# Optimization experiments

Hardware: AMD Instinct MI355X
Metric: run time of the kernel (lower is better)

## Reference

```python
import jax, jax.numpy as jnp
import numpy as np
from jax import lax

N, C, H, W = 16, 1024, 32, 32
CQK = C // 8
EPS = 1e-5


def setup_inputs() -> dict:
    key = jax.random.key(0)
    ks = jax.random.split(key, 10)
    s = lambda fan_in: 1.0 / np.sqrt(fan_in)
    return {
        "x": jax.random.normal(ks[0], (N, C, H, W), dtype=jnp.float32),
        "head_w": jax.random.uniform(ks[1], (1, C, 3, 3), jnp.float32, -s(C * 9), s(C * 9)),
        "bn_w": jnp.ones((1,), jnp.float32),
        "bn_b": jnp.zeros((1,), jnp.float32),
        "q_w": jax.random.uniform(ks[2], (CQK, C), jnp.float32, -s(C), s(C)),
        "q_b": jax.random.uniform(ks[3], (CQK,), jnp.float32, -s(C), s(C)),
        "k_w": jax.random.uniform(ks[4], (CQK, C), jnp.float32, -s(C), s(C)),
        "k_b": jax.random.uniform(ks[5], (CQK,), jnp.float32, -s(C), s(C)),
        "v_w": jax.random.uniform(ks[6], (C, C), jnp.float32, -s(C), s(C)),
        "v_b": jax.random.uniform(ks[7], (C,), jnp.float32, -s(C), s(C)),
        "gamma": jnp.ones((1,), jnp.float32),
    }


def reference(x, head_w, bn_w, bn_b, q_w, q_b, k_w, k_b, v_w, v_b, gamma):
    n, c, h, w = x.shape
    hw = h * w
    # activation head: 3x3 conv (no bias) -> BatchNorm (train mode, batch stats) -> sigmoid
    a = lax.conv_general_dilated(x, head_w, (1, 1), ((1, 1), (1, 1)),
                                 dimension_numbers=("NCHW", "OIHW", "NCHW"))  # [n,1,h,w]
    mu = jnp.mean(a, axis=(0, 2, 3), keepdims=True)
    var = jnp.mean((a - mu) ** 2, axis=(0, 2, 3), keepdims=True)
    bn = (a - mu) / jnp.sqrt(var + EPS) * bn_w.reshape(1, -1, 1, 1) + bn_b.reshape(1, -1, 1, 1)
    ccam = jax.nn.sigmoid(bn)  # [n,1,h,w]

    xf = x.reshape(n, c, hw)                 # [n,c,hw]
    cm = ccam.reshape(n, hw)                 # [n,hw]
    fg = jnp.einsum("nh,nch->nc", cm, xf) / hw
    bg = jnp.einsum("nh,nch->nc", 1.0 - cm, xf) / hw

    # self-attention with 1x1-conv projections (no 1/sqrt(d) scaling, per source)
    q = jnp.einsum("oc,nch->noh", q_w, xf) + q_b[None, :, None]  # [n,cqk,hw]
    k = jnp.einsum("oc,nch->noh", k_w, xf) + k_b[None, :, None]
    v = jnp.einsum("oc,nch->noh", v_w, xf) + v_b[None, :, None]  # [n,c,hw]
    attn = jax.nn.softmax(jnp.einsum("noi,noj->nij", q, k), axis=-1)  # [n,hw,hw]
    out = jnp.einsum("ncj,nij->nci", v, attn)                         # [n,c,hw]
    out = gamma * out + xf

    global_feats = jnp.max(out, axis=-1)  # adaptive_max_pool2d to (1,1)
    return fg, bg, ccam, global_feats
```

## Files before the change

### kernel.cpp

```cpp
#include <hip/hip_runtime.h>
#include <math.h>

typedef _Float16 f16x8 __attribute__((ext_vector_type(8)));
typedef float f32x4 __attribute__((ext_vector_type(4)));

#define NB 16
#define CC 1024
#define HW 1024
#define CQK 128
#define EPS 1e-5f

#define OFF_A     0
#define OFF_STATS 65536
#define OFF_CM    66048
#define OFF_WH    131584
#define OFF_QT    (OFF_WH + 2621440)
#define OFF_KT    (OFF_QT + 4194304)
#define OFF_V     (OFF_KT + 4194304)
#define OFF_XH    (OFF_V + 33554432)
#define OFF_ATTN  OFF_XH
#define OFF_PMAX  (OFF_ATTN + 67108864)
#define OFF_YP    OFF_V

__device__ __forceinline__ ushort f16b(float f) {
    union { _Float16 h; ushort u; } v;
    v.h = (_Float16)f;
    return v.u;
}

__device__ __forceinline__ void gl_lds16(const void* g, void* s) {
    __builtin_amdgcn_global_load_lds(
        (const __attribute__((address_space(1))) void*)g,
        (__attribute__((address_space(3))) void*)s, 16, 0, 0);
}

__global__ __launch_bounds__(256) void cvtT_x_conv(
        const float* __restrict__ x, const float* __restrict__ hwt,
        ushort* __restrict__ xh, float* __restrict__ yp) {
    int n = blockIdx.z, cb = blockIdx.y, hb = blockIdx.x;
    __shared__ float tile[32][33];
    int t = threadIdx.x;
    int r = t >> 3, c4 = (t & 7) << 2;
    const float* s = x + ((size_t)(n * CC + cb * 32 + r) << 10) + hb * 32 + c4;
    float4 v = *(const float4*)s;
    tile[r][c4] = v.x; tile[r][c4 + 1] = v.y; tile[r][c4 + 2] = v.z; tile[r][c4 + 3] = v.w;
    __syncthreads();
    int hw_l = t >> 3, cg = (t & 7) << 2;
    ushort4 h4;
    h4.x = f16b(tile[cg + 0][hw_l]); h4.y = f16b(tile[cg + 1][hw_l]);
    h4.z = f16b(tile[cg + 2][hw_l]); h4.w = f16b(tile[cg + 3][hw_l]);
    *(ushort4*)&xh[((size_t)(n * HW + hb * 32 + hw_l) << 10) + cb * 32 + cg] = h4;
    float pacc[9] = {};
    #pragma unroll
    for (int cc = 0; cc < 4; ++cc) {
        float xv = tile[cg + cc][hw_l];
        const float* w9 = hwt + (cb * 32 + cg + cc) * 9;
        #pragma unroll
        for (int tp = 0; tp < 9; ++tp) pacc[tp] += xv * w9[tp];
    }
    #pragma unroll
    for (int off = 1; off < 8; off <<= 1)
        #pragma unroll
        for (int tp = 0; tp < 9; ++tp) pacc[tp] += __shfl_xor(pacc[tp], off);
    if ((t & 7) == 0) {
        #pragma unroll
        for (int tp = 0; tp < 9; ++tp)
            yp[(((size_t)(n * 32 + cb) * 9 + tp) << 10) + hb * 32 + hw_l] = pacc[tp];
    }
}

__global__ __launch_bounds__(256) void conv_combine(
        const float* __restrict__ yp, float* __restrict__ a) {
    int idx = blockIdx.x * 256 + threadIdx.x;
    int n = idx >> 10, p = idx & 1023;
    int h = p >> 5, w = p & 31;
    float s = 0.f;
    #pragma unroll
    for (int tp = 0; tp < 9; ++tp) {
        int dy = tp / 3 - 1, dx = tp % 3 - 1;
        int hh = h + dy, ww = w + dx;
        if (hh < 0 || hh > 31 || ww < 0 || ww > 31) continue;
        int pp = (hh << 5) + ww;
        const float* b = yp + (((size_t)(n * 32) * 9) << 10) + ((size_t)tp << 10) + pp;
        #pragma unroll
        for (int cch = 0; cch < 32; ++cch) s += b[((size_t)cch * 9) << 10];
    }
    a[idx] = s;
}

__global__ void bn_stats(const float* __restrict__ a, float* __restrict__ stats) {
    int t = threadIdx.x;
    float s = 0.f, ss = 0.f;
    for (int i = t; i < NB * HW; i += 256) { float v = a[i]; s += v; ss += v * v; }
    __shared__ float rs[256], rss[256];
    rs[t] = s; rss[t] = ss;
    __syncthreads();
    for (int off = 128; off > 0; off >>= 1) {
        if (t < off) { rs[t] += rs[t + off]; rss[t] += rss[t + off]; }
        __syncthreads();
    }
    if (t == 0) {
        float mu = rs[0] / (NB * HW);
        float var = rss[0] / (NB * HW) - mu * mu;
        stats[0] = mu;
        stats[1] = rsqrtf(var + EPS);
    }
}

__global__ void ccam_kernel(const float* __restrict__ a, const float* __restrict__ stats,
                            const float* __restrict__ bn_w, const float* __restrict__ bn_b,
                            float* __restrict__ cm, float* __restrict__ out_ccam) {
    int i = blockIdx.x * 256 + threadIdx.x;
    float z = (a[i] - stats[0]) * stats[1] * bn_w[0] + bn_b[0];
    float sg = 1.f / (1.f + expf(-z));
    cm[i] = sg;
    out_ccam[i] = sg;
}

__global__ void fgbg_kernel(const float* __restrict__ x, const float* __restrict__ cm,
                            float* __restrict__ out_fg, float* __restrict__ out_bg) {
    int gid = blockIdx.x * blockDim.x + threadIdx.x;
    int wid = gid >> 6;
    int lane = threadIdx.x & 63;
    int n = wid >> 10, c = wid & 1023;
    const float4* xp = (const float4*)(x + ((size_t)(n * CC + c) << 10));
    const float4* cp = (const float4*)(cm + (n << 10));
    float sf = 0.f, sa = 0.f;
    #pragma unroll
    for (int it = 0; it < 4; ++it) {
        float4 xv = xp[lane + (it << 6)];
        float4 cv = cp[lane + (it << 6)];
        sf += xv.x * cv.x + xv.y * cv.y + xv.z * cv.z + xv.w * cv.w;
        sa += xv.x + xv.y + xv.z + xv.w;
    }
    for (int off = 32; off > 0; off >>= 1) { sf += __shfl_xor(sf, off); sa += __shfl_xor(sa, off); }
    if (lane == 0) {
        float fgv = sf * (1.f / HW);
        out_fg[(n << 10) + c] = fgv;
        out_bg[(n << 10) + c] = sa * (1.f / HW) - fgv;
    }
}

__global__ void cvt_w(const float* __restrict__ qw, const float* __restrict__ kw,
                      const float* __restrict__ vw, ushort* __restrict__ wh) {
    size_t e = ((size_t)blockIdx.x * 256 + threadIdx.x) * 4;
    float4 v;
    if (e < 131072)       v = *(const float4*)(qw + e);
    else if (e < 262144)  v = *(const float4*)(kw + e - 131072);
    else                  v = *(const float4*)(vw + e - 262144);
    ushort4 h4;
    h4.x = f16b(v.x); h4.y = f16b(v.y); h4.z = f16b(v.z); h4.w = f16b(v.w);
    *(ushort4*)&wh[e] = h4;
}

__device__ __forceinline__ void gemm_loop_f16(
        const ushort* __restrict__ Ag, int ap,
        const ushort* __restrict__ Bg, int bp,
        int K, ushort* lds, f32x4 acc[4][4]) {
    const int t = threadIdx.x;
    const int lane = t & 63, w = t >> 6;
    const int lr = lane & 15, kg = lane >> 4;
    const int wm = (w >> 1) << 6, wn = (w & 1) << 6;
    const int rowl = lane >> 3;
    const int cs = (lane & 7) ^ rowl;
    const ushort* sA = Ag + cs * 8;
    const ushort* sB = Bg + cs * 8;
    const int rb = (w << 3) + rowl;
    const int ldsb = w << 9;
    const int cA0 = kg ^ (lr & 7);
    const int cA1 = (kg | 4) ^ (lr & 7);
    const int nt = K >> 6;
    #pragma unroll
    for (int q = 0; q < 4; ++q) {
        int r = rb + (q << 5);
        gl_lds16(sA + (size_t)r * ap, lds + ldsb + (q << 11));
        gl_lds16(sB + (size_t)r * bp, lds + 8192 + ldsb + (q << 11));
    }
    __syncthreads();
    int buf = 0;
    for (int tile = 0; tile < nt; ++tile) {
        if (tile + 1 < nt) {
            int nb = (buf ^ 1) << 14;
            int k0 = (tile + 1) << 6;
            #pragma unroll
            for (int q = 0; q < 4; ++q) {
                int r = rb + (q << 5);
                gl_lds16(sA + (size_t)r * ap + k0, lds + nb + ldsb + (q << 11));
                gl_lds16(sB + (size_t)r * bp + k0, lds + nb + 8192 + ldsb + (q << 11));
            }
        }
        const ushort* Ab = lds + (buf << 14);
        const ushort* Bb = Ab + 8192;
        #pragma unroll
        for (int s = 0; s < 2; ++s) {
            int ch = s ? cA1 : cA0;
            f16x8 a[4], b[4];
            #pragma unroll
            for (int i = 0; i < 4; ++i) {
                a[i] = *(const f16x8*)&Ab[((wm + i * 16 + lr) << 6) + ch * 8];
                b[i] = *(const f16x8*)&Bb[((wn + i * 16 + lr) << 6) + ch * 8];
            }
            #pragma unroll
            for (int i = 0; i < 4; ++i)
                #pragma unroll
                for (int j = 0; j < 4; ++j)
                    acc[i][j] = __builtin_amdgcn_mfma_f32_16x16x32_f16(a[i], b[j], acc[i][j], 0, 0, 0);
        }
        __syncthreads();
        buf ^= 1;
    }
}

__global__ __launch_bounds__(256) void qkv_f16(
        const ushort* __restrict__ Wh, const ushort* __restrict__ xh,
        const float* __restrict__ qb, const float* __restrict__ kb,
        const float* __restrict__ vb,
        ushort* __restrict__ qt, ushort* __restrict__ kt, ushort* __restrict__ v) {
    __shared__ __align__(16) ushort lds[32768];
    int n = blockIdx.z, m0 = blockIdx.y << 7, j0 = blockIdx.x << 7;
    f32x4 acc[4][4];
    #pragma unroll
    for (int i = 0; i < 4; ++i)
        #pragma unroll
        for (int j = 0; j < 4; ++j) acc[i][j] = (f32x4){0.f, 0.f, 0.f, 0.f};
    gemm_loop_f16(Wh + (size_t)m0 * CC, CC,
                  xh + ((size_t)(n * HW + j0)) * CC, CC, CC, lds, acc);
    const int t = threadIdx.x, lane = t & 63, wid = t >> 6;
    const int lr = lane & 15, kg = lane >> 4;
    const int wm = (wid >> 1) << 6, wn = (wid & 1) << 6;
    if (m0 < 256) {
        ushort* dst = (m0 == 0) ? qt : kt;
        const float* bp = (m0 == 0) ? qb : kb;
        #pragma unroll
        for (int mi = 0; mi < 4; ++mi)
            #pragma unroll
            for (int nj = 0; nj < 4; ++nj) {
                int m = wm + mi * 16 + kg * 4;
                int j = j0 + wn + nj * 16 + lr;
                ushort4 pk;
                pk.x = f16b(acc[mi][nj][0] + bp[m + 0]);
                pk.y = f16b(acc[mi][nj][1] + bp[m + 1]);
                pk.z = f16b(acc[mi][nj][2] + bp[m + 2]);
                pk.w = f16b(acc[mi][nj][3] + bp[m + 3]);
                *(ushort4*)&dst[((size_t)(n * HW + j) << 7) + m] = pk;
            }
    } else {
        int mo = m0 - 256;
        __syncthreads();
        #pragma unroll
        for (int mi = 0; mi < 4; ++mi)
            #pragma unroll
            for (int nj = 0; nj < 4; ++nj) {
                int ml = wm + mi * 16 + kg * 4;
                int jl = wn + nj * 16 + lr;
                #pragma unroll
                for (int r = 0; r < 4; ++r)
                    lds[(ml + r) * 136 + jl] = f16b(acc[mi][nj][r] + vb[mo + ml + r]);
            }
        __syncthreads();
        #pragma unroll
        for (int p = 0; p < 8; ++p) {
            int row = (t >> 4) + p * 16;
            int ch = (t & 15) * 8;
            *(uint4*)&v[((size_t)(n * CC + mo + row) << 10) + j0 + ch] =
                *(const uint4*)&lds[row * 136 + ch];
        }
    }
}

__global__ __launch_bounds__(256) void score_f16(
        const ushort* __restrict__ qt, const ushort* __restrict__ kt,
        float* __restrict__ attn) {
    __shared__ __align__(16) ushort lds[32768];
    int n = blockIdx.z, i0 = blockIdx.y << 7, j0 = blockIdx.x << 7;
    f32x4 acc[4][4];
    #pragma unroll
    for (int i = 0; i < 4; ++i)
        #pragma unroll
        for (int j = 0; j < 4; ++j) acc[i][j] = (f32x4){0.f, 0.f, 0.f, 0.f};
    gemm_loop_f16(qt + ((size_t)(n * HW + i0)) * CQK, CQK,
                  kt + ((size_t)(n * HW + j0)) * CQK, CQK, CQK, lds, acc);
    const int t = threadIdx.x, lane = t & 63, wid = t >> 6;
    const int lr = lane & 15, kg = lane >> 4;
    const int wm = (wid >> 1) << 6, wn = (wid & 1) << 6;
    #pragma unroll
    for (int mi = 0; mi < 4; ++mi)
        #pragma unroll
        for (int r = 0; r < 4; ++r) {
            int irow = i0 + wm + mi * 16 + kg * 4 + r;
            #pragma unroll
            for (int nj = 0; nj < 4; ++nj) {
                int j = j0 + wn + nj * 16 + lr;
                attn[((size_t)(n * HW + irow) << 10) + j] = acc[mi][nj][r];
            }
        }
}

__global__ void softmax_f16(float* __restrict__ attn) {
    int row = blockIdx.x;
    float* p = attn + ((size_t)row << 10);
    int t = threadIdx.x;
    int wid = t >> 6, lane = t & 63;
    float4 v4 = *(const float4*)&p[t << 2];
    float m = fmaxf(fmaxf(v4.x, v4.y), fmaxf(v4.z, v4.w));
    for (int off = 32; off > 0; off >>= 1) m = fmaxf(m, __shfl_xor(m, off));
    __shared__ float redm[4], reds[4];
    if (lane == 0) redm[wid] = m;
    __syncthreads();
    if (t == 0) {
        float mm = fmaxf(fmaxf(redm[0], redm[1]), fmaxf(redm[2], redm[3]));
        redm[0] = mm;
    }
    __syncthreads();
    m = redm[0];
    v4.x = expf(v4.x - m); v4.y = expf(v4.y - m);
    v4.z = expf(v4.z - m); v4.w = expf(v4.w - m);
    float s = v4.x + v4.y + v4.z + v4.w;
    for (int off = 32; off > 0; off >>= 1) s += __shfl_xor(s, off);
    if (lane == 0) reds[wid] = s;
    __syncthreads();
    if (t == 0) reds[0] = reds[0] + reds[1] + reds[2] + reds[3];
    __syncthreads();
    float inv = 1.f / reds[0];
    ushort4 h4;
    h4.x = f16b(v4.x * inv); h4.y = f16b(v4.y * inv);
    h4.z = f16b(v4.z * inv); h4.w = f16b(v4.w * inv);
    *(ushort4*)&((ushort*)p)[t << 2] = h4;
}

__global__ __launch_bounds__(256) void out_f16(
        const ushort* __restrict__ v, const ushort* __restrict__ pus,
        const float* __restrict__ x, const float* __restrict__ gamma,
        float* __restrict__ pmax) {
    __shared__ __align__(16) ushort lds[32768];
    int n = blockIdx.z, c0 = blockIdx.y << 7, i0 = blockIdx.x << 7;
    f32x4 acc[4][4];
    #pragma unroll
    for (int i = 0; i < 4; ++i)
        #pragma unroll
        for (int j = 0; j < 4; ++j) acc[i][j] = (f32x4){0.f, 0.f, 0.f, 0.f};
    gemm_loop_f16(v + ((size_t)(n * CC + c0) << 10), HW,
                  pus + ((size_t)(n * HW + i0)) * 2048, 2048, HW, lds, acc);
    const int t = threadIdx.x, lane = t & 63, wid = t >> 6;
    const int lr = lane & 15, kg = lane >> 4;
    const int wm = (wid >> 1) << 6, wn = (wid & 1) << 6;
    float g = gamma[0];
    __syncthreads();
    float (*smax)[64] = (float(*)[64])lds;
    #pragma unroll
    for (int mi = 0; mi < 4; ++mi)
        #pragma unroll
        for (int r = 0; r < 4; ++r) {
            int c = c0 + wm + mi * 16 + kg * 4 + r;
            const float* xp = x + ((size_t)(n * CC + c) << 10);
            float mx = -INFINITY;
            #pragma unroll
            for (int nj = 0; nj < 4; ++nj) {
                int i = i0 + wn + nj * 16 + lr;
                mx = fmaxf(mx, g * acc[mi][nj][r] + xp[i]);
            }
            #pragma unroll
            for (int off = 1; off < 16; off <<= 1) mx = fmaxf(mx, __shfl_xor(mx, off));
            if (lr == 0) smax[wid][mi * 16 + kg * 4 + r] = mx;
        }
    __syncthreads();
    if (t < 128) {
        int half = t >> 6, cl = t & 63;
        float m = fmaxf(smax[half * 2][cl], smax[half * 2 + 1][cl]);
        pmax[((size_t)(n * 8 + blockIdx.x) << 10) + c0 + half * 64 + cl] = m;
    }
}

__global__ void gf_reduce(const float* __restrict__ pmax, float* __restrict__ gf) {
    int idx = blockIdx.x * 256 + threadIdx.x;
    int n = idx >> 10, c = idx & 1023;
    float m = -INFINITY;
    #pragma unroll
    for (int ib = 0; ib < 8; ++ib)
        m = fmaxf(m, pmax[(((size_t)(n << 3) + ib) << 10) + c]);
    gf[idx] = m;
}

extern "C" void kernel_launch(void* const* d_in, const int* in_sizes, int n_in,
                              void* d_out, int out_size, void* d_ws, size_t ws_size,
                              hipStream_t stream) {
    const float* x      = (const float*)d_in[0];
    const float* head_w = (const float*)d_in[1];
    const float* bn_w   = (const float*)d_in[2];
    const float* bn_b   = (const float*)d_in[3];
    const float* q_w    = (const float*)d_in[4];
    const float* q_b    = (const float*)d_in[5];
    const float* k_w    = (const float*)d_in[6];
    const float* k_b    = (const float*)d_in[7];
    const float* v_w    = (const float*)d_in[8];
    const float* v_b    = (const float*)d_in[9];
    const float* gamma  = (const float*)d_in[10];

    float* out      = (float*)d_out;
    float* out_fg   = out;
    float* out_bg   = out + 16384;
    float* out_ccam = out + 32768;
    float* out_gf   = out + 49152;

    char* B = (char*)d_ws;
    float*  a     = (float*)(B + OFF_A);
    float*  stats = (float*)(B + OFF_STATS);
    float*  cm    = (float*)(B + OFF_CM);
    ushort* Wh    = (ushort*)(B + OFF_WH);
    ushort* qt    = (ushort*)(B + OFF_QT);
    ushort* kt    = (ushort*)(B + OFF_KT);
    ushort* v     = (ushort*)(B + OFF_V);
    ushort* xh    = (ushort*)(B + OFF_XH);
    float*  attn  = (float*)(B + OFF_ATTN);
    float*  pmax  = (float*)(B + OFF_PMAX);
    float*  ypart = (float*)(B + OFF_YP);

    hipLaunchKernelGGL(cvtT_x_conv, dim3(32, 32, 16), dim3(256), 0, stream, x, head_w, xh, ypart);
    hipLaunchKernelGGL(conv_combine, dim3(64), dim3(256), 0, stream, ypart, a);
    hipLaunchKernelGGL(bn_stats, dim3(1), dim3(256), 0, stream, a, stats);
    hipLaunchKernelGGL(ccam_kernel, dim3(64), dim3(256), 0, stream, a, stats, bn_w, bn_b, cm, out_ccam);
    hipLaunchKernelGGL(fgbg_kernel, dim3(4096), dim3(256), 0, stream, x, cm, out_fg, out_bg);

    hipLaunchKernelGGL(cvt_w, dim3(1280), dim3(256), 0, stream, q_w, k_w, v_w, Wh);
    hipLaunchKernelGGL(qkv_f16, dim3(8, 10, 16), dim3(256), 0, stream,
                       Wh, xh, q_b, k_b, v_b, qt, kt, v);
    hipLaunchKernelGGL(score_f16, dim3(8, 8, 16), dim3(256), 0, stream, qt, kt, attn);
    hipLaunchKernelGGL(softmax_f16, dim3(NB * HW), dim3(256), 0, stream, attn);
    hipLaunchKernelGGL(out_f16, dim3(8, 8, 16), dim3(256), 0, stream,
                       v, (const ushort*)attn, x, gamma, pmax);
    hipLaunchKernelGGL(gf_reduce, dim3(64), dim3(256), 0, stream, pmax, out_gf);
}
```

Measured before the change: 336.7 us.

## Load GEMM A operand directly from global memory, stage only B in LDS

The shared f16 GEMM loop now reads the A operand fragments straight from global memory into registers, using per-row pointers. Only B is double-buffered through LDS. This halves LDS use in the qkv, score and out kernels, which is meant to raise occupancy and cut LDS write and read traffic. The cost is that A loads are no longer prefetched a tile ahead, so global latency sits on the MFMA critical path. Each A row is also fetched by two waves and served from the caches rather than shared through LDS.

```diff
diff --git a/kernel.cpp b/kernel.cpp
--- a/kernel.cpp
+++ b/kernel.cpp
@@ -163,41 +163,38 @@
     const int wm = (w >> 1) << 6, wn = (w & 1) << 6;
     const int rowl = lane >> 3;
     const int cs = (lane & 7) ^ rowl;
-    const ushort* sA = Ag + cs * 8;
     const ushort* sB = Bg + cs * 8;
     const int rb = (w << 3) + rowl;
     const int ldsb = w << 9;
-    const int cA0 = kg ^ (lr & 7);
-    const int cA1 = (kg | 4) ^ (lr & 7);
+    const int cB0 = kg ^ (lr & 7);
+    const int cB1 = (kg | 4) ^ (lr & 7);
+    const ushort* arow[4];
+    #pragma unroll
+    for (int i = 0; i < 4; ++i)
+        arow[i] = Ag + (size_t)(wm + i * 16 + lr) * ap + kg * 8;
     const int nt = K >> 6;
     #pragma unroll
-    for (int q = 0; q < 4; ++q) {
-        int r = rb + (q << 5);
-        gl_lds16(sA + (size_t)r * ap, lds + ldsb + (q << 11));
-        gl_lds16(sB + (size_t)r * bp, lds + 8192 + ldsb + (q << 11));
-    }
+    for (int q = 0; q < 4; ++q)
+        gl_lds16(sB + (size_t)(rb + (q << 5)) * bp, lds + ldsb + (q << 11));
     __syncthreads();
     int buf = 0;
     for (int tile = 0; tile < nt; ++tile) {
         if (tile + 1 < nt) {
-            int nb = (buf ^ 1) << 14;
+            int nb = (buf ^ 1) << 13;
             int k0 = (tile + 1) << 6;
             #pragma unroll
-            for (int q = 0; q < 4; ++q) {
-                int r = rb + (q << 5);
-                gl_lds16(sA + (size_t)r * ap + k0, lds + nb + ldsb + (q << 11));
-                gl_lds16(sB + (size_t)r * bp + k0, lds + nb + 8192 + ldsb + (q << 11));
-            }
+            for (int q = 0; q < 4; ++q)
+                gl_lds16(sB + (size_t)(rb + (q << 5)) * bp + k0, lds + nb + ldsb + (q << 11));
         }
-        const ushort* Ab = lds + (buf << 14);
-        const ushort* Bb = Ab + 8192;
+        const ushort* Bb = lds + (buf << 13);
+        int kbase = tile << 6;
         #pragma unroll
         for (int s = 0; s < 2; ++s) {
-            int ch = s ? cA1 : cA0;
+            int ch = s ? cB1 : cB0;
             f16x8 a[4], b[4];
             #pragma unroll
             for (int i = 0; i < 4; ++i) {
-                a[i] = *(const f16x8*)&Ab[((wm + i * 16 + lr) << 6) + ch * 8];
+                a[i] = *(const f16x8*)&arow[i][kbase + (s << 5)];
                 b[i] = *(const f16x8*)&Bb[((wn + i * 16 + lr) << 6) + ch * 8];
             }
             #pragma unroll
@@ -216,7 +213,7 @@
         const float* __restrict__ qb, const float* __restrict__ kb,
         const float* __restrict__ vb,
         ushort* __restrict__ qt, ushort* __restrict__ kt, ushort* __restrict__ v) {
-    __shared__ __align__(16) ushort lds[32768];
+    __shared__ __align__(16) ushort lds[17408];
     int n = blockIdx.z, m0 = blockIdx.y << 7, j0 = blockIdx.x << 7;
     f32x4 acc[4][4];
     #pragma unroll
@@ -271,7 +268,7 @@
 __global__ __launch_bounds__(256) void score_f16(
         const ushort* __restrict__ qt, const ushort* __restrict__ kt,
         float* __restrict__ attn) {
-    __shared__ __align__(16) ushort lds[32768];
+    __shared__ __align__(16) ushort lds[16384];
     int n = blockIdx.z, i0 = blockIdx.y << 7, j0 = blockIdx.x << 7;
     f32x4 acc[4][4];
     #pragma unroll
@@ -332,7 +329,7 @@
         const ushort* __restrict__ v, const ushort* __restrict__ pus,
         const float* __restrict__ x, const float* __restrict__ gamma,
         float* __restrict__ pmax) {
-    __shared__ __align__(16) ushort lds[32768];
+    __shared__ __align__(16) ushort lds[16384];
     int n = blockIdx.z, c0 = blockIdx.y << 7, i0 = blockIdx.x << 7;
     f32x4 acc[4][4];
     #pragma unroll
```

Result: slower. 431.0 us (+28.0%).
